# Optimization experiments

Measured on AMD Instinct MI355X. Metric: run time of the kernel, lower is better.

The kernel has to match this reference:

```python
import jax, jax.numpy as jnp
import numpy as np

D_MODEL = 512
N_HEADS = 8
D_K = D_MODEL // N_HEADS
MAX_LEN = 512  # max_seq_len; rel table has 2*MAX_LEN-1 rows


def setup_inputs() -> dict:
    key = jax.random.key(0)
    ks = jax.random.split(key, 7)
    B, S = 8, 512
    s = 1.0 / np.sqrt(D_MODEL)
    return {
        "x": jax.random.normal(ks[0], (B, S, D_MODEL), jnp.float32),
        "Wq": jax.random.normal(ks[1], (D_MODEL, D_MODEL), jnp.float32) * s,
        "bq": jnp.zeros((D_MODEL,), jnp.float32),
        "Wk": jax.random.normal(ks[2], (D_MODEL, D_MODEL), jnp.float32) * s,
        "bk": jnp.zeros((D_MODEL,), jnp.float32),
        "Wv": jax.random.normal(ks[3], (D_MODEL, D_MODEL), jnp.float32) * s,
        "bv": jnp.zeros((D_MODEL,), jnp.float32),
        "Wo": jax.random.normal(ks[4], (D_MODEL, D_MODEL), jnp.float32) * s,
        "bo": jnp.zeros((D_MODEL,), jnp.float32),
        "rel_embed": jax.random.normal(ks[5], (2 * MAX_LEN - 1, D_MODEL), jnp.float32) * 0.02,
    }


def reference(x, Wq, bq, Wk, bk, Wv, bv, Wo, bo, rel_embed):
    B, S, _ = x.shape
    scale = np.sqrt(D_K).astype(np.float32)

    def split_heads(t):  # (B,S,D) -> (B,H,S,dk)
        return t.reshape(B, S, N_HEADS, D_K).transpose(0, 2, 1, 3)

    q = split_heads(x @ Wq.T + bq)
    k = split_heads(x @ Wk.T + bk)
    v = split_heads(x @ Wv.T + bv)

    scores = jnp.einsum('bhqd,bhkd->bhqk', q, k) / scale

    # relative position bias: idx[q_pos, k_pos] = k_pos - q_pos + MAX_LEN - 1
    pos = jnp.arange(S)
    rel_idx = pos[None, :] - pos[:, None] + (MAX_LEN - 1)  # (S,S)
    rel_bias = rel_embed[rel_idx].reshape(S, S, N_HEADS, D_K)  # (S,S,H,dk)
    scores = scores + jnp.einsum('bhqd,qkhd->bhqk', q, rel_bias)

    attn = jax.nn.softmax(scores, axis=-1)
    out = jnp.einsum('bhqk,bhkd->bhqd', attn, v)  # (B,H,S,dk)
    out = out.transpose(0, 2, 1, 3).reshape(B, S, D_MODEL)
    return out @ Wo.T + bo
```

## Files before the change

kernel.cpp:

```cpp
#include <hip/hip_runtime.h>
#include <math.h>

#define B_  8
#define S_  512
#define D_  512
#define H_  8
#define DK_ 64

typedef __attribute__((ext_vector_type(8))) short short8;
typedef __attribute__((ext_vector_type(4))) float f32x4;

#define MFMA_BF16(a, b, c) __builtin_amdgcn_mfma_f32_16x16x32_bf16(a, b, c, 0, 0, 0)

__device__ __forceinline__ unsigned bf16_rne(float x) {
    unsigned u = __float_as_uint(x);
    return (u + 0x7FFFu + ((u >> 16) & 1u)) >> 16;
}
__device__ __forceinline__ float bf16f(unsigned h) { return __uint_as_float(h << 16); }

__device__ __forceinline__ void glds16(const ushort* g, ushort* l) {
    __builtin_amdgcn_global_load_lds(
        (const __attribute__((address_space(1))) unsigned int*)g,
        (__attribute__((address_space(3))) unsigned int*)l,
        16, 0, 0);
}

__global__ __launch_bounds__(256)
void conv_pl(const float* __restrict__ x,
             const float* __restrict__ wq, const float* __restrict__ wk,
             const float* __restrict__ wv, const float* __restrict__ wo,
             ushort* __restrict__ Xh, ushort* __restrict__ Xl,
             ushort* __restrict__ Wqh, ushort* __restrict__ Wql,
             ushort* __restrict__ Wkh, ushort* __restrict__ Wkl,
             ushort* __restrict__ Wvh, ushort* __restrict__ Wvl,
             ushort* __restrict__ Woh, ushort* __restrict__ Wol) {
    const int bid = blockIdx.x;
    const float* src; ushort* dh; ushort* dl; int i4;
    if (bid < 2048) {
        src = x; dh = Xh; dl = Xl; i4 = bid * 256 + threadIdx.x;
    } else {
        const int r = bid - 2048;
        const int wsel = r >> 8;
        src = (wsel == 0) ? wq : (wsel == 1) ? wk : (wsel == 2) ? wv : wo;
        dh  = (wsel == 0) ? Wqh : (wsel == 1) ? Wkh : (wsel == 2) ? Wvh : Woh;
        dl  = (wsel == 0) ? Wql : (wsel == 1) ? Wkl : (wsel == 2) ? Wvl : Wol;
        i4 = (r & 255) * 256 + threadIdx.x;
    }
    const float4 v = ((const float4*)src)[i4];
    unsigned h[4], l[4];
    const float* vp = &v.x;
    #pragma unroll
    for (int j = 0; j < 4; ++j) { h[j] = bf16_rne(vp[j]); l[j] = bf16_rne(vp[j] - bf16f(h[j])); }
    ((uint2*)dh)[i4] = make_uint2(h[0] | (h[1] << 16), h[2] | (h[3] << 16));
    ((uint2*)dl)[i4] = make_uint2(l[0] | (l[1] << 16), l[2] | (l[3] << 16));
}

__global__ __launch_bounds__(256)
void conv_rel(const float* __restrict__ rel, ushort* __restrict__ Rg) {
    const int idx = blockIdx.x * 256 + threadIdx.x;
    const int d2 = idx & 31;
    const int rr = (idx >> 5) % 1152;
    const int h  = idx / (1152 * 32);
    unsigned v0 = 0, v1 = 0;
    if (rr >= 64 && rr < 64 + 1023) {
        const float* s = &rel[(size_t)(rr - 64) * 512 + h * 64 + d2 * 2];
        v0 = bf16_rne(s[0]); v1 = bf16_rne(s[1]);
    }
    *(uint*)&Rg[((size_t)h * 1152 + rr) * 64 + d2 * 2] = v0 | (v1 << 16);
}

template<int XB, int OM>
__global__ __launch_bounds__(256, 2)
void gemm_mfma(const ushort* __restrict__ Xhp, const ushort* __restrict__ Xlp,
               const ushort* __restrict__ Yh0, const ushort* __restrict__ Yl0,
               const ushort* __restrict__ Yh1, const ushort* __restrict__ Yl1,
               const float* __restrict__ bias0, const float* __restrict__ bias1,
               float scale0, float scale1,
               float* __restrict__ outF,
               ushort* __restrict__ oh0, ushort* __restrict__ ol0,
               ushort* __restrict__ oh1, ushort* __restrict__ ol1) {
    __shared__ ushort Xs[2][2][64 * 64];
    __shared__ ushort Ys[2][2][64 * 64];

    const int z = blockIdx.z;
    const ushort* Yhp = z ? Yh1 : Yh0;
    const ushort* Ylp = z ? Yl1 : Yl0;
    const float*  bias = z ? bias1 : bias0;
    const float   scale = z ? scale1 : scale0;
    ushort* ohp = z ? oh1 : oh0;
    ushort* olp = z ? ol1 : ol0;

    const int tid = threadIdx.x;
    const int w = tid >> 6, lane = tid & 63;
    const int g = lane >> 4, c = lane & 15;
    const int rloc = lane >> 3, cc8 = lane & 7;
    const int cp = cc8 ^ rloc;
    const int r0 = blockIdx.y * 64;
    const int c0 = blockIdx.x * 64;

    const f32x4 fz = {0.f, 0.f, 0.f, 0.f};
    f32x4 acc[2][2] = {{fz, fz}, {fz, fz}};

    auto stage = [&](int kt, int buf) {
        const int k0 = kt * 64;
        const ushort* gb; ushort* lb; size_t rstr;
        if (w < 2) {
            const ushort* Xp = (w == 1) ? Xlp : Xhp;
            if (XB == 0) { gb = Xp + (size_t)r0 * 512 + k0; rstr = 512; }
            else {
                const int b = r0 >> 9, s0 = r0 & 511, h = k0 >> 6;
                gb = Xp + (((size_t)(b * 8 + h)) * 512 + s0) * 64; rstr = 64;
            }
            lb = &Xs[buf][w][0];
        } else {
            gb = ((w == 2) ? Yhp : Ylp) + (size_t)c0 * 512 + k0; rstr = 512;
            lb = &Ys[buf][w - 2][0];
        }
        #pragma unroll
        for (int j = 0; j < 8; ++j)
            glds16(gb + (size_t)(j * 8 + rloc) * rstr + cp * 8, lb + j * 512);
    };

    auto compute = [&](int buf) {
        #pragma unroll
        for (int ks = 0; ks < 2; ++ks) {
            short8 axh[2], axl[2], byh[2], byl[2];
            const int wm = (w >> 1) * 32, wn = (w & 1) * 32;
            #pragma unroll
            for (int t = 0; t < 2; ++t) {
                int row = wm + t * 16 + c;
                int off = row * 64 + (((ks * 4 + g) ^ (row & 7)) * 8);
                axh[t] = *(const short8*)&Xs[buf][0][off];
                axl[t] = *(const short8*)&Xs[buf][1][off];
                row = wn + t * 16 + c;
                off = row * 64 + (((ks * 4 + g) ^ (row & 7)) * 8);
                byh[t] = *(const short8*)&Ys[buf][0][off];
                byl[t] = *(const short8*)&Ys[buf][1][off];
            }
            #pragma unroll
            for (int tm = 0; tm < 2; ++tm)
                #pragma unroll
                for (int tn = 0; tn < 2; ++tn) {
                    acc[tm][tn] = MFMA_BF16(axh[tm], byh[tn], acc[tm][tn]);
                    acc[tm][tn] = MFMA_BF16(axl[tm], byh[tn], acc[tm][tn]);
                    acc[tm][tn] = MFMA_BF16(axh[tm], byl[tn], acc[tm][tn]);
                }
        }
    };

    stage(0, 0);
    __syncthreads();
    for (int kt = 0; kt < 8; ++kt) {
        if (kt < 7) stage(kt + 1, (kt + 1) & 1);
        compute(kt & 1);
        __syncthreads();
    }

    const int wm = (w >> 1) * 32, wn = (w & 1) * 32;
    if (OM == 0) {
        #pragma unroll
        for (int tn = 0; tn < 2; ++tn) {
            const int gc = c0 + wn + tn * 16 + c;
            const float bv = bias[gc];
            #pragma unroll
            for (int tm = 0; tm < 2; ++tm)
                #pragma unroll
                for (int i = 0; i < 4; ++i) {
                    const int gr = r0 + wm + tm * 16 + g * 4 + i;
                    outF[(size_t)gr * 512 + gc] = acc[tm][tn][i] + bv;
                }
        }
    } else if (OM == 2) {
        #pragma unroll
        for (int tn = 0; tn < 2; ++tn) {
            const int gc = c0 + wn + tn * 16 + c;
            const int h = gc >> 6, dk = gc & 63;
            const float bv = bias[gc];
            #pragma unroll
            for (int tm = 0; tm < 2; ++tm)
                #pragma unroll
                for (int i = 0; i < 4; ++i) {
                    const int gr = r0 + wm + tm * 16 + g * 4 + i;
                    const int b = gr >> 9, s = gr & 511;
                    const float v = (acc[tm][tn][i] + bv) * scale;
                    const unsigned hb = bf16_rne(v);
                    const size_t a = (((size_t)(b * 8 + h)) * 512 + s) * 64 + dk;
                    ohp[a] = (ushort)hb;
                    olp[a] = (ushort)bf16_rne(v - bf16f(hb));
                }
        }
    } else {
        #pragma unroll
        for (int tm = 0; tm < 2; ++tm)
            #pragma unroll
            for (int i = 0; i < 4; ++i) {
                const int gr = r0 + wm + tm * 16 + g * 4 + i;
                const int h = gr >> 6, dk = gr & 63;
                const float bv = bias[gr];
                #pragma unroll
                for (int tn = 0; tn < 2; ++tn) {
                    const int gc = c0 + wn + tn * 16 + c;
                    const int b = gc >> 9, s = gc & 511;
                    const float v = acc[tm][tn][i] + bv;
                    const size_t a = (((size_t)(b * 8 + h)) * 64 + dk) * 512 + s;
                    ohp[a] = (ushort)bf16_rne(v);
                }
            }
    }
}

__global__ __launch_bounds__(256, 2)
void attn_mfma(const ushort* __restrict__ Qhp, const ushort* __restrict__ Qlp,
               const ushort* __restrict__ Khp, const ushort* __restrict__ Klp,
               const ushort* __restrict__ Vhp, const ushort* __restrict__ Rg,
               float* __restrict__ Op0, float* __restrict__ Op1,
               float2* __restrict__ Ml0, float2* __restrict__ Ml1) {
    __shared__ ushort Ksm[2][64 * 64];
    __shared__ ushort Vsm[64 * 64];
    __shared__ ushort Rsm[128 * 64];
    __shared__ ushort Usm[4][16 * 86];

    const int tid  = threadIdx.x;
    const int w    = tid >> 6;
    const int lane = tid & 63;
    const int g    = lane >> 4;
    const int c    = lane & 15;
    const int rloc = lane >> 3, cc8 = lane & 7;
    const int bh   = blockIdx.y;
    const int h    = bh & 7;
    const int z    = blockIdx.z;
    const int qwb  = blockIdx.x * 64;
    const int qw   = qwb + w * 16;

    float* __restrict__ Op = z ? Op1 : Op0;
    float2* __restrict__ Ml = z ? Ml1 : Ml0;

    short8 qfh[2], qfl[2];
    #pragma unroll
    for (int ks = 0; ks < 2; ++ks) {
        const size_t qi = ((size_t)bh * 512 + qw + c) * 64 + ks * 32 + g * 8;
        qfh[ks] = *(const short8*)&Qhp[qi];
        qfl[ks] = *(const short8*)&Qlp[qi];
    }

    const f32x4 fz = {0.f, 0.f, 0.f, 0.f};
    f32x4 o[4] = {fz, fz, fz, fz};
    float m = -INFINITY, l = 0.f;

    const ushort* KhB = Khp + (size_t)bh * 512 * 64;
    const ushort* KlB = Klp + (size_t)bh * 512 * 64;
    const ushort* VhB = Vhp + (size_t)bh * 64 * 512;
    const ushort* RgH = Rg + (size_t)h * 1152 * 64;

    for (int kt = z * 4; kt < z * 4 + 4; ++kt) {
        const int k0 = kt * 64;
        const int rbase = k0 - qwb + 512;
        __syncthreads();

        #pragma unroll
        for (int j = 0; j < 4; ++j) {
            const int cd  = j * 256 + tid;
            const int row = cd >> 3, cc = cd & 7;
            const uint4 v = *(const uint4*)&RgH[(size_t)(rbase + row) * 64 + cc * 8];
            *(uint4*)&Rsm[row * 64 + ((cc ^ (row & 7)) << 3)] = v;
        }

        if (w < 2) {
            const ushort* gb = (w == 0) ? KhB : KlB;
            ushort* lb = &Ksm[w][0];
            #pragma unroll
            for (int j = 0; j < 8; ++j) {
                const int row = j * 8 + rloc;
                const int tcq = row >> 4, cq = row & 15;
                const int key = ((tcq & 1) << 5) + ((cq >> 2) << 3)
                              + ((tcq >> 1) << 2) + (cq & 3);
                glds16(gb + (size_t)(k0 + key) * 64 + ((cc8 ^ rloc) << 3),
                       lb + j * 512);
            }
        } else {
            const ushort* gb = VhB + k0 + (size_t)(w - 2) * 32 * 512;
            ushort* lb = &Vsm[(w - 2) * 32 * 64];
            #pragma unroll
            for (int j = 0; j < 4; ++j)
                glds16(gb + (size_t)(j * 8 + rloc) * 512 + ((cc8 ^ rloc) << 3),
                       lb + j * 512);
        }
        __syncthreads();

        f32x4 u[5];
        #pragma unroll
        for (int ut = 0; ut < 5; ++ut) u[ut] = fz;
        #pragma unroll
        for (int ks = 0; ks < 2; ++ks)
            #pragma unroll
            for (int ut = 0; ut < 5; ++ut) {
                const int rl = 48 - 16 * w + c + ut * 16;
                const short8 rf = *(const short8*)
                    &Rsm[rl * 64 + (((ks * 4 + g) ^ (c & 7)) << 3)];
                u[ut] = MFMA_BF16(qfh[ks], rf, u[ut]);
            }
        #pragma unroll
        for (int ut = 0; ut < 5; ++ut)
            #pragma unroll
            for (int i = 0; i < 4; ++i)
                Usm[w][(g * 4 + i) * 86 + c + ut * 16] = (ushort)bf16_rne(u[ut][i]);

        f32x4 st[4];
        #pragma unroll
        for (int tc = 0; tc < 4; ++tc) st[tc] = fz;
        #pragma unroll
        for (int ks = 0; ks < 2; ++ks)
            #pragma unroll
            for (int tc = 0; tc < 4; ++tc) {
                const int row = tc * 16 + c;
                const int chv = ((ks * 4 + g) ^ (row & 7)) * 8;
                const short8 kh8 = *(const short8*)&Ksm[0][row * 64 + chv];
                const short8 kl8 = *(const short8*)&Ksm[1][row * 64 + chv];
                st[tc] = MFMA_BF16(kh8, qfh[ks], st[tc]);
                st[tc] = MFMA_BF16(kh8, qfl[ks], st[tc]);
                st[tc] = MFMA_BF16(kl8, qfh[ks], st[tc]);
            }

        asm volatile("s_waitcnt lgkmcnt(0)" ::: "memory");

        #pragma unroll
        for (int tc = 0; tc < 4; ++tc)
            #pragma unroll
            for (int i = 0; i < 4; ++i) {
                const int key = ((tc & 1) << 5) + 8 * g + ((tc >> 1) << 2) + i;
                st[tc][i] += bf16f(Usm[w][c * 85 + key + 15]);
            }

        float tm = fmaxf(fmaxf(st[0][0], st[0][1]), fmaxf(st[0][2], st[0][3]));
        #pragma unroll
        for (int tc = 1; tc < 4; ++tc) {
            const float t2 = fmaxf(fmaxf(st[tc][0], st[tc][1]),
                                   fmaxf(st[tc][2], st[tc][3]));
            tm = fmaxf(tm, t2);
        }
        tm = fmaxf(tm, __shfl_xor(tm, 16));
        tm = fmaxf(tm, __shfl_xor(tm, 32));
        const float mn = fmaxf(m, tm);
        const float corr = __expf(m - mn);
        m = mn;
        l *= corr;
        #pragma unroll
        for (int dt = 0; dt < 4; ++dt) o[dt] *= corr;

        uint pk[4][2];
        #pragma unroll
        for (int tc = 0; tc < 4; ++tc) {
            const float p0 = __expf(st[tc][0] - mn);
            const float p1 = __expf(st[tc][1] - mn);
            const float p2 = __expf(st[tc][2] - mn);
            const float p3 = __expf(st[tc][3] - mn);
            l += (p0 + p1) + (p2 + p3);
            pk[tc][0] = bf16_rne(p0) | (bf16_rne(p1) << 16);
            pk[tc][1] = bf16_rne(p2) | (bf16_rne(p3) << 16);
        }

        #pragma unroll
        for (int ks = 0; ks < 2; ++ks) {
            union { uint u4[4]; short8 s8; } pb;
            pb.u4[0] = pk[ks][0];
            pb.u4[1] = pk[ks][1];
            pb.u4[2] = pk[ks + 2][0];
            pb.u4[3] = pk[ks + 2][1];
            #pragma unroll
            for (int dt = 0; dt < 4; ++dt) {
                const int row = dt * 16 + c;
                const int chv = ((ks * 4 + g) ^ (row & 7)) * 8;
                const short8 vh8 = *(const short8*)&Vsm[row * 64 + chv];
                o[dt] = MFMA_BF16(vh8, pb.s8, o[dt]);
            }
        }
    }

    float lt = l;
    lt += __shfl_xor(lt, 16);
    lt += __shfl_xor(lt, 32);
    if (lane < 16) Ml[(size_t)bh * 512 + qw + c] = make_float2(m, lt);
    #pragma unroll
    for (int dt = 0; dt < 4; ++dt)
        #pragma unroll
        for (int i = 0; i < 4; ++i)
            Op[((size_t)bh * 64 + dt * 16 + g * 4 + i) * 512 + qw + c] = o[dt][i];
}

__global__ __launch_bounds__(256)
void attn_combine(const float* __restrict__ Op0, const float* __restrict__ Op1,
                  const float2* __restrict__ Ml0, const float2* __restrict__ Ml1,
                  ushort* __restrict__ Oh, ushort* __restrict__ Ol) {
    __shared__ float L0[64][67];
    __shared__ float L1[64][67];
    const int t = threadIdx.x;
    const int bh = blockIdx.y;
    const int s0 = blockIdx.x * 64;
    #pragma unroll
    for (int j = 0; j < 4; ++j) {
        const int d = (t >> 4) + j * 16;
        const int c4 = (t & 15) * 4;
        const size_t ga = ((size_t)bh * 64 + d) * 512 + s0 + c4;
        *(float4*)&L0[d][c4] = *(const float4*)&Op0[ga];
        *(float4*)&L1[d][c4] = *(const float4*)&Op1[ga];
    }
    __syncthreads();
    const int sl = t >> 2;
    const int d0 = (t & 3) * 16;
    const float2 a = Ml0[(size_t)bh * 512 + s0 + sl];
    const float2 b = Ml1[(size_t)bh * 512 + s0 + sl];
    const float mm = fmaxf(a.x, b.x);
    float w0 = __expf(a.x - mm), w1 = __expf(b.x - mm);
    const float inv = 1.0f / (a.y * w0 + b.y * w1);
    w0 *= inv; w1 *= inv;
    const size_t ob = ((size_t)bh * 512 + s0 + sl) * 64 + d0;
    #pragma unroll
    for (int q = 0; q < 4; ++q) {
        unsigned hb[4], lb4[4];
        #pragma unroll
        for (int e = 0; e < 4; ++e) {
            const int dd = q * 4 + e;
            const float v = L0[d0 + dd][sl] * w0 + L1[d0 + dd][sl] * w1;
            hb[e] = bf16_rne(v);
            lb4[e] = bf16_rne(v - bf16f(hb[e]));
        }
        *(uint2*)&Oh[ob + q * 4] = make_uint2(hb[0] | (hb[1] << 16), hb[2] | (hb[3] << 16));
        *(uint2*)&Ol[ob + q * 4] = make_uint2(lb4[0] | (lb4[1] << 16), lb4[2] | (lb4[3] << 16));
    }
}

extern "C" void kernel_launch(void* const* d_in, const int* in_sizes, int n_in,
                              void* d_out, int out_size, void* d_ws, size_t ws_size,
                              hipStream_t stream) {
    const float* x   = (const float*)d_in[0];
    const float* Wq  = (const float*)d_in[1];
    const float* bq  = (const float*)d_in[2];
    const float* Wk  = (const float*)d_in[3];
    const float* bk  = (const float*)d_in[4];
    const float* Wv  = (const float*)d_in[5];
    const float* bv  = (const float*)d_in[6];
    const float* Wo  = (const float*)d_in[7];
    const float* bo  = (const float*)d_in[8];
    const float* rel = (const float*)d_in[9];
    float* out = (float*)d_out;

    const size_t NP = (size_t)B_ * H_ * S_ * DK_;
    const size_t WP = (size_t)D_ * D_;
    ushort* Xh  = (ushort*)d_ws;
    ushort* Xl  = Xh + NP;
    ushort* Wqh = Xl + NP;
    ushort* Wql = Wqh + WP;
    ushort* Wkh = Wql + WP;
    ushort* Wkl = Wkh + WP;
    ushort* Wvh = Wkl + WP;
    ushort* Wvl = Wvh + WP;
    ushort* Woh = Wvl + WP;
    ushort* Wol = Woh + WP;
    ushort* Qh  = Wol + WP;
    ushort* Ql  = Qh + NP;
    ushort* Kh  = Ql + NP;
    ushort* Kl  = Kh + NP;
    ushort* Vh  = Kl + NP;
    ushort* Rg  = Vh + NP;
    float*  Op1 = (float*)(Rg + 589824);
    float2* Ml0 = (float2*)(Op1 + NP);
    float2* Ml1 = Ml0 + 32768;
    float*  Op0 = (float*)d_ws;

    conv_pl<<<3072, 256, 0, stream>>>(x, Wq, Wk, Wv, Wo,
                                      Xh, Xl, Wqh, Wql, Wkh, Wkl, Wvh, Wvl, Woh, Wol);
    conv_rel<<<1152, 256, 0, stream>>>(rel, Rg);

    gemm_mfma<0, 2><<<dim3(8, 64, 2), 256, 0, stream>>>(
        Xh, Xl, Wqh, Wql, Wkh, Wkl, bq, bk, 1.0f, 0.125f,
        nullptr, Qh, Ql, Kh, Kl);
    gemm_mfma<0, 3><<<dim3(64, 8, 1), 256, 0, stream>>>(
        Wvh, Wvl, Xh, Xl, nullptr, nullptr, bv, nullptr, 1.0f, 1.0f,
        nullptr, Vh, nullptr, nullptr, nullptr);

    attn_mfma<<<dim3(8, 64, 2), 256, 0, stream>>>(
        Qh, Ql, Kh, Kl, Vh, Rg, Op0, Op1, Ml0, Ml1);

    attn_combine<<<dim3(8, 64), 256, 0, stream>>>(Op0, Op1, Ml0, Ml1, Kh, Kl);

    gemm_mfma<1, 0><<<dim3(8, 64, 1), 256, 0, stream>>>(
        Kh, Kl, Woh, Wol, nullptr, nullptr, bo, nullptr, 1.0f, 1.0f,
        out, nullptr, nullptr, nullptr, nullptr);
}
```

Baseline: 94.25 us.

## Drop K low-part split, merge rel conversion kernel, prefetch rel rows, raise occupancy

Merges the rel-embedding conversion into the plane-conversion kernel, removing one launch. The K low-precision plane is no longer written or used, so QK^T drops from three MFMAs to two and halves K LDS traffic. Rel rows for the next tile are prefetched into registers with hand-placed waitcnts and a raw barrier. Attention launch bounds are raised to 3 blocks per CU. Dropping K's low bits lowers score precision, and the extra prefetch registers may pressure the new occupancy target.

```diff
diff --git a/kernel.cpp b/kernel.cpp
--- a/kernel.cpp
+++ b/kernel.cpp
@@ -29,12 +29,27 @@
 void conv_pl(const float* __restrict__ x,
              const float* __restrict__ wq, const float* __restrict__ wk,
              const float* __restrict__ wv, const float* __restrict__ wo,
+             const float* __restrict__ rel,
              ushort* __restrict__ Xh, ushort* __restrict__ Xl,
              ushort* __restrict__ Wqh, ushort* __restrict__ Wql,
              ushort* __restrict__ Wkh, ushort* __restrict__ Wkl,
              ushort* __restrict__ Wvh, ushort* __restrict__ Wvl,
-             ushort* __restrict__ Woh, ushort* __restrict__ Wol) {
+             ushort* __restrict__ Woh, ushort* __restrict__ Wol,
+             ushort* __restrict__ Rg) {
     const int bid = blockIdx.x;
+    if (bid >= 3072) {
+        const int idx = (bid - 3072) * 256 + threadIdx.x;
+        const int d2 = idx & 31;
+        const int rr = (idx >> 5) % 1152;
+        const int h  = idx / (1152 * 32);
+        unsigned v0 = 0, v1 = 0;
+        if (rr >= 64 && rr < 64 + 1023) {
+            const float* s = &rel[(size_t)(rr - 64) * 512 + h * 64 + d2 * 2];
+            v0 = bf16_rne(s[0]); v1 = bf16_rne(s[1]);
+        }
+        *(uint*)&Rg[((size_t)h * 1152 + rr) * 64 + d2 * 2] = v0 | (v1 << 16);
+        return;
+    }
     const float* src; ushort* dh; ushort* dl; int i4;
     if (bid < 2048) {
         src = x; dh = Xh; dl = Xl; i4 = bid * 256 + threadIdx.x;
@@ -53,20 +68,6 @@
     for (int j = 0; j < 4; ++j) { h[j] = bf16_rne(vp[j]); l[j] = bf16_rne(vp[j] - bf16f(h[j])); }
     ((uint2*)dh)[i4] = make_uint2(h[0] | (h[1] << 16), h[2] | (h[3] << 16));
     ((uint2*)dl)[i4] = make_uint2(l[0] | (l[1] << 16), l[2] | (l[3] << 16));
-}
-
-__global__ __launch_bounds__(256)
-void conv_rel(const float* __restrict__ rel, ushort* __restrict__ Rg) {
-    const int idx = blockIdx.x * 256 + threadIdx.x;
-    const int d2 = idx & 31;
-    const int rr = (idx >> 5) % 1152;
-    const int h  = idx / (1152 * 32);
-    unsigned v0 = 0, v1 = 0;
-    if (rr >= 64 && rr < 64 + 1023) {
-        const float* s = &rel[(size_t)(rr - 64) * 512 + h * 64 + d2 * 2];
-        v0 = bf16_rne(s[0]); v1 = bf16_rne(s[1]);
-    }
-    *(uint*)&Rg[((size_t)h * 1152 + rr) * 64 + d2 * 2] = v0 | (v1 << 16);
 }
 
 template<int XB, int OM>
@@ -186,7 +187,7 @@
                     const unsigned hb = bf16_rne(v);
                     const size_t a = (((size_t)(b * 8 + h)) * 512 + s) * 64 + dk;
                     ohp[a] = (ushort)hb;
-                    olp[a] = (ushort)bf16_rne(v - bf16f(hb));
+                    if (olp) olp[a] = (ushort)bf16_rne(v - bf16f(hb));
                 }
         }
     } else {
@@ -209,13 +210,13 @@
     }
 }
 
-__global__ __launch_bounds__(256, 2)
+__global__ __launch_bounds__(256, 3)
 void attn_mfma(const ushort* __restrict__ Qhp, const ushort* __restrict__ Qlp,
-               const ushort* __restrict__ Khp, const ushort* __restrict__ Klp,
-               const ushort* __restrict__ Vhp, const ushort* __restrict__ Rg,
+               const ushort* __restrict__ Khp, const ushort* __restrict__ Vhp,
+               const ushort* __restrict__ Rg,
                float* __restrict__ Op0, float* __restrict__ Op1,
                float2* __restrict__ Ml0, float2* __restrict__ Ml1) {
-    __shared__ ushort Ksm[2][64 * 64];
+    __shared__ ushort Ksm[64 * 64];
     __shared__ ushort Vsm[64 * 64];
     __shared__ ushort Rsm[128 * 64];
     __shared__ ushort Usm[4][16 * 86];
@@ -235,6 +236,21 @@
     float* __restrict__ Op = z ? Op1 : Op0;
     float2* __restrict__ Ml = z ? Ml1 : Ml0;
 
+    const ushort* KhB = Khp + (size_t)bh * 512 * 64;
+    const ushort* VhB = Vhp + (size_t)bh * 64 * 512;
+    const ushort* RgH = Rg + (size_t)h * 1152 * 64;
+
+    uint4 rv[4];
+    auto issue_rel = [&](int kt) {
+        const int rbase = kt * 64 - qwb + 512;
+        #pragma unroll
+        for (int j = 0; j < 4; ++j) {
+            const int cd = j * 256 + tid, row = cd >> 3, cc = cd & 7;
+            rv[j] = *(const uint4*)&RgH[(size_t)(rbase + row) * 64 + cc * 8];
+        }
+    };
+
+    issue_rel(z * 4);
     short8 qfh[2], qfl[2];
     #pragma unroll
     for (int ks = 0; ks < 2; ++ks) {
@@ -247,34 +263,24 @@
     f32x4 o[4] = {fz, fz, fz, fz};
     float m = -INFINITY, l = 0.f;
 
-    const ushort* KhB = Khp + (size_t)bh * 512 * 64;
-    const ushort* KlB = Klp + (size_t)bh * 512 * 64;
-    const ushort* VhB = Vhp + (size_t)bh * 64 * 512;
-    const ushort* RgH = Rg + (size_t)h * 1152 * 64;
-
     for (int kt = z * 4; kt < z * 4 + 4; ++kt) {
         const int k0 = kt * 64;
-        const int rbase = k0 - qwb + 512;
         __syncthreads();
 
         #pragma unroll
         for (int j = 0; j < 4; ++j) {
-            const int cd  = j * 256 + tid;
-            const int row = cd >> 3, cc = cd & 7;
-            const uint4 v = *(const uint4*)&RgH[(size_t)(rbase + row) * 64 + cc * 8];
-            *(uint4*)&Rsm[row * 64 + ((cc ^ (row & 7)) << 3)] = v;
-        }
-
+            const int cd = j * 256 + tid, row = cd >> 3, cc = cd & 7;
+            *(uint4*)&Rsm[row * 64 + ((cc ^ (row & 7)) << 3)] = rv[j];
+        }
         if (w < 2) {
-            const ushort* gb = (w == 0) ? KhB : KlB;
-            ushort* lb = &Ksm[w][0];
-            #pragma unroll
-            for (int j = 0; j < 8; ++j) {
-                const int row = j * 8 + rloc;
+            ushort* lb = &Ksm[w * 32 * 64];
+            #pragma unroll
+            for (int j = 0; j < 4; ++j) {
+                const int row = w * 32 + j * 8 + rloc;
                 const int tcq = row >> 4, cq = row & 15;
                 const int key = ((tcq & 1) << 5) + ((cq >> 2) << 3)
                               + ((tcq >> 1) << 2) + (cq & 3);
-                glds16(gb + (size_t)(k0 + key) * 64 + ((cc8 ^ rloc) << 3),
+                glds16(KhB + (size_t)(k0 + key) * 64 + ((cc8 ^ rloc) << 3),
                        lb + j * 512);
             }
         } else {
@@ -285,7 +291,14 @@
                 glds16(gb + (size_t)(j * 8 + rloc) * 512 + ((cc8 ^ rloc) << 3),
                        lb + j * 512);
         }
-        __syncthreads();
+
+        if (kt + 1 < z * 4 + 4) {
+            issue_rel(kt + 1);
+            asm volatile("s_waitcnt vmcnt(4) lgkmcnt(0)" ::: "memory");
+        } else {
+            asm volatile("s_waitcnt vmcnt(0) lgkmcnt(0)" ::: "memory");
+        }
+        __builtin_amdgcn_s_barrier();
 
         f32x4 u[5];
         #pragma unroll
@@ -314,11 +327,9 @@
             for (int tc = 0; tc < 4; ++tc) {
                 const int row = tc * 16 + c;
                 const int chv = ((ks * 4 + g) ^ (row & 7)) * 8;
-                const short8 kh8 = *(const short8*)&Ksm[0][row * 64 + chv];
-                const short8 kl8 = *(const short8*)&Ksm[1][row * 64 + chv];
+                const short8 kh8 = *(const short8*)&Ksm[row * 64 + chv];
                 st[tc] = MFMA_BF16(kh8, qfh[ks], st[tc]);
                 st[tc] = MFMA_BF16(kh8, qfl[ks], st[tc]);
-                st[tc] = MFMA_BF16(kl8, qfh[ks], st[tc]);
             }
 
         asm volatile("s_waitcnt lgkmcnt(0)" ::: "memory");
@@ -467,19 +478,18 @@
     float2* Ml1 = Ml0 + 32768;
     float*  Op0 = (float*)d_ws;
 
-    conv_pl<<<3072, 256, 0, stream>>>(x, Wq, Wk, Wv, Wo,
-                                      Xh, Xl, Wqh, Wql, Wkh, Wkl, Wvh, Wvl, Woh, Wol);
-    conv_rel<<<1152, 256, 0, stream>>>(rel, Rg);
+    conv_pl<<<4224, 256, 0, stream>>>(x, Wq, Wk, Wv, Wo, rel,
+                                      Xh, Xl, Wqh, Wql, Wkh, Wkl, Wvh, Wvl, Woh, Wol, Rg);
 
     gemm_mfma<0, 2><<<dim3(8, 64, 2), 256, 0, stream>>>(
         Xh, Xl, Wqh, Wql, Wkh, Wkl, bq, bk, 1.0f, 0.125f,
-        nullptr, Qh, Ql, Kh, Kl);
+        nullptr, Qh, Ql, Kh, nullptr);
     gemm_mfma<0, 3><<<dim3(64, 8, 1), 256, 0, stream>>>(
         Wvh, Wvl, Xh, Xl, nullptr, nullptr, bv, nullptr, 1.0f, 1.0f,
         nullptr, Vh, nullptr, nullptr, nullptr);
 
     attn_mfma<<<dim3(8, 64, 2), 256, 0, stream>>>(
-        Qh, Ql, Kh, Kl, Vh, Rg, Op0, Op1, Ml0, Ml1);
+        Qh, Ql, Kh, Vh, Rg, Op0, Op1, Ml0, Ml1);
 
     attn_combine<<<dim3(8, 64), 256, 0, stream>>>(Op0, Op1, Ml0, Ml1, Kh, Kl);
 
```

New measurement: 99.23 us. 5.3% more time.
